# Optimization experiments

Hardware: AMD Instinct MI355X
Metric: run time of the kernel (lower is better)

## Reference

```python
import jax, jax.numpy as jnp
import numpy as np

N_NODES = 100_000
N_FACES = 200_000
N_EDGES1 = 800_000
N_TRIP = 500_000
H = 64
GEO_IN = 10 + 2 * 23  # 56
N_INTER = 3
DEPTH = 3  # finaldepth; total SPNN layers = DEPTH + 1
PI = float(np.pi)
EPS = 1e-5


def setup_inputs() -> dict:
    key = jax.random.key(0)
    ks = jax.random.split(key, 12)
    s = 0.05
    input_feature = jax.random.normal(ks[0], (N_NODES, H), jnp.float32)
    coords = jax.random.normal(ks[1], (N_NODES, 3), jnp.float32)
    face_norm = jax.random.normal(ks[2], (N_FACES, 3), jnp.float32)
    face_x = jax.random.normal(ks[3], (N_FACES, 23), jnp.float32)
    edge_whichface = jax.random.randint(ks[4], (N_EDGES1,), 0, N_FACES)
    edge_index_2rd = jax.random.randint(ks[5], (3, N_TRIP), 0, N_NODES)
    edx_ij = jax.random.randint(ks[6], (N_TRIP,), 0, N_EDGES1)
    edx_rand = jax.random.randint(ks[7], (N_TRIP,), 0, N_EDGES1)
    edx_jk = jnp.where(jnp.arange(N_TRIP) % 2 == 0, edx_ij, edx_rand)
    att = jnp.ones((2,), jnp.float32)
    W_geo = jax.random.normal(ks[8], (H, GEO_IN), jnp.float32) * s
    b_geo = jnp.zeros((H,), jnp.float32)
    g_geo = jnp.ones((H,), jnp.float32)
    be_geo = jnp.zeros((H,), jnp.float32)
    spnn_W0 = jax.random.normal(ks[9], (N_INTER, 2, H, 4 * H), jnp.float32) * s
    spnn_b0 = jnp.zeros((N_INTER, 2, H), jnp.float32)
    spnn_Wr = jax.random.normal(ks[10], (N_INTER, 2, DEPTH, H, H), jnp.float32) * s
    spnn_br = jnp.zeros((N_INTER, 2, DEPTH, H), jnp.float32)
    bn_g = jnp.ones((N_INTER, 2, DEPTH + 1, H), jnp.float32)
    bn_b = jnp.zeros((N_INTER, 2, DEPTH + 1, H), jnp.float32)
    return dict(input_feature=input_feature, coords=coords, face_norm=face_norm,
                face_x=face_x, att=att, W_geo=W_geo, b_geo=b_geo, g_geo=g_geo,
                be_geo=be_geo, spnn_W0=spnn_W0, spnn_b0=spnn_b0, spnn_Wr=spnn_Wr,
                spnn_br=spnn_br, bn_g=bn_g, bn_b=bn_b,
                edge_whichface=edge_whichface, edge_index_2rd=edge_index_2rd,
                edx_jk=edx_jk, edx_ij=edx_ij)


def _bn(x, g, b):
    # BatchNorm1d, training mode (batch stats, biased variance)
    mean = x.mean(0)
    var = ((x - mean) ** 2).mean(0)
    return (x - mean) * jax.lax.rsqrt(var + EPS) * g + b


def _masked_bn(x, mf, g, b):
    # BatchNorm over only the masked rows (original code runs BN on x_i[mask]);
    # applied to all rows, masked rows selected afterward -> identical math.
    cnt = jnp.maximum(mf.sum(), 1.0)
    mean = (x * mf).sum(0) / cnt
    var = (((x - mean) ** 2) * mf).sum(0) / cnt
    return (x - mean) * jax.lax.rsqrt(var + EPS) * g + b


def _angle(v1, v2):
    c = jnp.cross(v1, v2)
    return jnp.arctan2(jnp.linalg.norm(c, axis=1), (v1 * v2).sum(1))


def reference(input_feature, coords, face_norm, face_x, att, W_geo, b_geo,
              g_geo, be_geo, spnn_W0, spnn_b0, spnn_Wr, spnn_br, bn_g, bn_b,
              edge_whichface, edge_index_2rd, edx_jk, edx_ij):
    i, j, k = edge_index_2rd
    f_ij = edge_whichface[edx_ij]
    f_jk = edge_whichface[edx_jk]
    # angle_face is computed then multiplied by 0 in the original
    angle_face = (PI - _angle(face_norm[f_ij], face_norm[f_jk])) * 0.0
    cj, ci, ck = coords[j], coords[i], coords[k]
    d_ij = jnp.linalg.norm(cj - ci, axis=1)
    d_jk = jnp.linalg.norm(cj - ck, axis=1)
    theta = _angle(cj - ci, ck - cj)
    same_face = f_ij == f_jk
    geo = jnp.concatenate([d_ij[:, None], d_jk[:, None], theta[:, None],
                           angle_face[:, None], cj, ci,
                           face_x[f_ij], face_x[f_jk]], axis=-1)  # [E, 56]
    geo = jax.nn.relu(_bn(geo @ W_geo.T + b_geo, g_geo, be_geo))  # [E, H]

    nf = input_feature
    masks = [same_face, ~same_face]
    outs = []
    for t in range(N_INTER):
        xcat = jnp.concatenate([nf[i], nf[j], nf[k], geo], axis=-1)  # [E, 4H]
        x_out = jnp.zeros((xcat.shape[0], H), xcat.dtype)
        for bi in range(2):
            mf = masks[bi].astype(xcat.dtype)[:, None]
            x = jax.nn.relu(_masked_bn(xcat @ spnn_W0[t, bi].T + spnn_b0[t, bi],
                                       mf, bn_g[t, bi, 0], bn_b[t, bi, 0]))
            for l in range(DEPTH):
                x = jax.nn.relu(_masked_bn(x @ spnn_Wr[t, bi, l].T + spnn_br[t, bi, l],
                                           mf, bn_g[t, bi, l + 1], bn_b[t, bi, l + 1]))
            x = jax.nn.leaky_relu(x) * att[bi]
            x_out = x_out + x * mf
        nf = jax.ops.segment_sum(x_out, i, num_segments=N_NODES)
        outs.append(nf)
    return jnp.stack(outs)  # [N_INTER, N, H] (list in original)
```

## Files before the change

### kernel.cpp

```cpp
#include <hip/hip_runtime.h>

#define E_TRIP 500000
#define EPAD   500224
#define NTILE64 (EPAD/64)
#define NBLK256 (EPAD/256)
#define NBLK    1954
#define NN 100000
#define NBIN (2*NN)
#define EPSF 1e-5f
#define RSTAT 64

typedef _Float16 f16;
typedef _Float16 f16x8 __attribute__((ext_vector_type(8)));
typedef float f32x4 __attribute__((ext_vector_type(4)));

__global__ __launch_bounds__(256) void k_count(const int* __restrict__ ewf,
    const int* __restrict__ exij, const int* __restrict__ exjk,
    unsigned char* __restrict__ biedge, int* __restrict__ cb0)
{
  __shared__ int wcnt[4];
  int e = blockIdx.x*256 + threadIdx.x;
  bool active = e < E_TRIP;
  int b = 0;
  if (active) {
    int fij = ewf[exij[e]];
    int fjk = ewf[exjk[e]];
    b = (fij == fjk) ? 0 : 1;
    biedge[e] = (unsigned char)b;
  }
  unsigned long long m0 = __ballot(active && b==0);
  int lane = threadIdx.x & 63, wv = threadIdx.x >> 6;
  if (lane == 0) wcnt[wv] = (int)__popcll(m0);
  __syncthreads();
  if (threadIdx.x == 0) cb0[blockIdx.x] = wcnt[0] + wcnt[1] + wcnt[2] + wcnt[3];
}

__global__ __launch_bounds__(1024) void k_scanb(const int* __restrict__ cb0, int* __restrict__ sc)
{
  __shared__ int s[2048];
  int tid = threadIdx.x;
  int i0 = tid, i1 = tid + 1024;
  s[i0] = (i0 < NBLK) ? cb0[i0] : 0;
  s[i1] = (i1 < NBLK) ? cb0[i1] : 0;
  __syncthreads();
  for (int off = 1; off < 2048; off <<= 1) {
    int v0 = (i0 >= off) ? s[i0 - off] : 0;
    int v1 = (i1 >= off) ? s[i1 - off] : 0;
    __syncthreads();
    s[i0] += v0; s[i1] += v1;
    __syncthreads();
  }
  if (tid == 0) {
    int c0 = s[NBLK-1];
    int c0p = (c0 + 63) & ~63;
    sc[4] = c0; sc[5] = c0p; sc[6] = E_TRIP - c0;
  }
}

__global__ __launch_bounds__(256) void k_cvt(const float* __restrict__ W0,
    const float* __restrict__ Wr, const float* __restrict__ nf,
    f16* __restrict__ W0h, f16* __restrict__ Wrh, f16* __restrict__ nfh)
{
  int i = (blockIdx.x*256 + threadIdx.x) * 4;
  if (i < 98304) {
    float4 v = *(const float4*)(W0 + i);
    W0h[i]=(f16)v.x; W0h[i+1]=(f16)v.y; W0h[i+2]=(f16)v.z; W0h[i+3]=(f16)v.w;
  } else if (i < 172032) {
    int j = i - 98304;
    float4 v = *(const float4*)(Wr + j);
    Wrh[j]=(f16)v.x; Wrh[j+1]=(f16)v.y; Wrh[j+2]=(f16)v.z; Wrh[j+3]=(f16)v.w;
  } else {
    int j = i - 172032;
    if (j < NN*64) {
      float4 v = *(const float4*)(nf + j);
      nfh[j]=(f16)v.x; nfh[j+1]=(f16)v.y; nfh[j+2]=(f16)v.z; nfh[j+3]=(f16)v.w;
    }
  }
}

__global__ __launch_bounds__(256) void k_hist(const unsigned char* __restrict__ biedge,
    const int* __restrict__ eidx, int* __restrict__ cnt)
{
  int e = blockIdx.x*256 + threadIdx.x;
  if (e < E_TRIP) {
    int key = (int)biedge[e]*NN + eidx[e];
    atomicAdd(&cnt[key], 1);
  }
}

__global__ __launch_bounds__(512) void k_scan1(const int* __restrict__ cnt,
    int* __restrict__ start, int* __restrict__ btot)
{
  __shared__ int s[512];
  int tid = threadIdx.x;
  int g = blockIdx.x*512 + tid;
  int x = (g < NBIN) ? cnt[g] : 0;
  s[tid] = x; __syncthreads();
  #pragma unroll
  for (int off = 1; off < 512; off <<= 1) {
    int v = (tid >= off) ? s[tid-off] : 0;
    __syncthreads();
    s[tid] += v;
    __syncthreads();
  }
  if (g < NBIN) start[g] = s[tid] - x;
  if (tid == 511) btot[blockIdx.x] = s[511];
}

__global__ __launch_bounds__(512) void k_scan2(int* __restrict__ btot)
{
  __shared__ int s[512];
  int tid = threadIdx.x;
  int x = (tid < 391) ? btot[tid] : 0;
  s[tid] = x; __syncthreads();
  #pragma unroll
  for (int off = 1; off < 512; off <<= 1) {
    int v = (tid >= off) ? s[tid-off] : 0;
    __syncthreads();
    s[tid] += v;
    __syncthreads();
  }
  if (tid < 391) btot[tid] = s[tid] - x;
}

__global__ __launch_bounds__(512) void k_scan3(int* __restrict__ start,
    int* __restrict__ cur, const int* __restrict__ btot, const int* __restrict__ sc)
{
  int tid = threadIdx.x;
  int g = blockIdx.x*512 + tid;
  if (g < NBIN) {
    int v = start[g] + btot[blockIdx.x];
    if (g >= NN) v += sc[5] - sc[4];
    start[g] = v;
    cur[g] = v;
  }
  if (g == 0) start[NBIN] = sc[5] + sc[6];
}

__global__ __launch_bounds__(256) void k_place(const unsigned char* __restrict__ biedge,
    const int* __restrict__ eidx, int* __restrict__ cur,
    int* __restrict__ epos, int* __restrict__ ip, int* __restrict__ jp, int* __restrict__ kp)
{
  int e = blockIdx.x*256 + threadIdx.x;
  if (e < E_TRIP) {
    int i = eidx[e];
    int key = (int)biedge[e]*NN + i;
    int pos = atomicAdd(&cur[key], 1);
    epos[pos] = e;
    ip[pos] = i;
    jp[pos] = eidx[E_TRIP + e];
    kp[pos] = eidx[2*E_TRIP + e];
  }
}

__global__ __launch_bounds__(256) void k_geo(
    const float* __restrict__ coords, const float* __restrict__ facex,
    const int* __restrict__ ewf, const int* __restrict__ exij, const int* __restrict__ exjk,
    const float* __restrict__ Wgeo, const float* __restrict__ bgeo,
    const int* __restrict__ sc, const int* __restrict__ epos,
    const int* __restrict__ ip, const int* __restrict__ jp, const int* __restrict__ kp,
    f16* __restrict__ zgeo, float* __restrict__ gstats)
{
  __shared__ f16 lds[256*72];
  __shared__ float sstat[64][2];
  int tid = threadIdx.x;
  int base = blockIdx.x*256;
  int c0 = sc[4], c0p = sc[5], c1 = sc[6];
  if (tid < 128) ((float*)sstat)[tid] = 0.f;
  {
    int p = base + tid;
    bool valid = (p < c0) || (p >= c0p && p < c0p + c1);
    f16* lrow = lds + tid*72;
    if (valid) {
      int e = epos[p];
      int ii = ip[p], jj = jp[p], kk = kp[p];
      float cix = coords[ii*3+0], ciy = coords[ii*3+1], ciz = coords[ii*3+2];
      float cjx = coords[jj*3+0], cjy = coords[jj*3+1], cjz = coords[jj*3+2];
      float ckx = coords[kk*3+0], cky = coords[kk*3+1], ckz = coords[kk*3+2];
      float v1x = cjx-cix, v1y = cjy-ciy, v1z = cjz-ciz;
      float v2x = ckx-cjx, v2y = cky-cjy, v2z = ckz-cjz;
      float dij = sqrtf(v1x*v1x + v1y*v1y + v1z*v1z);
      float djk = sqrtf(v2x*v2x + v2y*v2y + v2z*v2z);
      float cx = v1y*v2z - v1z*v2y;
      float cy = v1z*v2x - v1x*v2z;
      float cz = v1x*v2y - v1y*v2x;
      float theta = atan2f(sqrtf(cx*cx+cy*cy+cz*cz), v1x*v2x+v1y*v2y+v1z*v2z);
      lrow[0]=(f16)dij; lrow[1]=(f16)djk; lrow[2]=(f16)theta; lrow[3]=(f16)0.f;
      lrow[4]=(f16)cjx; lrow[5]=(f16)cjy; lrow[6]=(f16)cjz;
      lrow[7]=(f16)cix; lrow[8]=(f16)ciy; lrow[9]=(f16)ciz;
      int fij = ewf[exij[e]], fjk = ewf[exjk[e]];
      const float* fx1 = facex + (size_t)fij*23;
      const float* fx2 = facex + (size_t)fjk*23;
      for (int c = 0; c < 23; c++) lrow[10+c] = (f16)fx1[c];
      for (int c = 0; c < 23; c++) lrow[33+c] = (f16)fx2[c];
      for (int c = 56; c < 64; c++) lrow[c] = (f16)0.f;
    } else {
      for (int c = 0; c < 64; c++) lrow[c] = (f16)0.f;
    }
  }
  __syncthreads();
  int wv = tid>>6, lane = tid&63, lg = lane>>4, lr = lane&15;
  f16x8 Bf[4][2];
  #pragma unroll
  for (int nt = 0; nt < 4; nt++) {
    #pragma unroll
    for (int ks = 0; ks < 2; ks++) {
      int n = nt*16 + lr;
      int kb = ks*32 + lg*8;
      f16x8 w;
      if (kb < 56) {
        float4 w0 = *(const float4*)(Wgeo + n*56 + kb);
        float4 w1 = *(const float4*)(Wgeo + n*56 + kb + 4);
        w[0]=(f16)w0.x; w[1]=(f16)w0.y; w[2]=(f16)w0.z; w[3]=(f16)w0.w;
        w[4]=(f16)w1.x; w[5]=(f16)w1.y; w[6]=(f16)w1.z; w[7]=(f16)w1.w;
      } else {
        #pragma unroll
        for (int j2 = 0; j2 < 8; j2++) w[j2] = (f16)0.f;
      }
      Bf[nt][ks] = w;
    }
  }
  float ssum[4] = {0,0,0,0}, ssq[4] = {0,0,0,0};
  for (int mt = 0; mt < 4; mt++) {
    int rbase = wv*64 + mt*16;
    f16x8 A0 = *(const f16x8*)(lds + (rbase+lr)*72 + lg*8);
    f16x8 A1 = *(const f16x8*)(lds + (rbase+lr)*72 + 32 + lg*8);
    f32x4 acc[4];
    #pragma unroll
    for (int nt = 0; nt < 4; nt++) { acc[nt][0]=0.f; acc[nt][1]=0.f; acc[nt][2]=0.f; acc[nt][3]=0.f; }
    #pragma unroll
    for (int nt = 0; nt < 4; nt++) {
      acc[nt] = __builtin_amdgcn_mfma_f32_16x16x32_f16(A0, Bf[nt][0], acc[nt], 0, 0, 0);
      acc[nt] = __builtin_amdgcn_mfma_f32_16x16x32_f16(A1, Bf[nt][1], acc[nt], 0, 0, 0);
    }
    #pragma unroll
    for (int nt = 0; nt < 4; nt++) {
      int n = nt*16 + lr;
      float bg = bgeo[n];
      #pragma unroll
      for (int rg = 0; rg < 4; rg++) {
        int rloc = rbase + lg*4 + rg;
        int p = base + rloc;
        bool valid = (p < c0) || (p >= c0p && p < c0p + c1);
        float z = valid ? (acc[nt][rg] + bg) : 0.f;
        ssum[nt] += z; ssq[nt] += z*z;
        lds[rloc*72 + n] = (f16)z;
      }
    }
  }
  #pragma unroll
  for (int nt = 0; nt < 4; nt++) {
    float v = ssum[nt]; v += __shfl_xor(v, 16); v += __shfl_xor(v, 32);
    float w = ssq[nt];  w += __shfl_xor(w, 16); w += __shfl_xor(w, 32);
    if (lane < 16) { atomicAdd(&sstat[nt*16+lane][0], v); atomicAdd(&sstat[nt*16+lane][1], w); }
  }
  __syncthreads();
  {
    int p = base + tid;
    #pragma unroll
    for (int c = 0; c < 8; c++) {
      f16x8 v = *(const f16x8*)(lds + tid*72 + c*8);
      *(f16x8*)(zgeo + (size_t)p*64 + c*8) = v;
    }
  }
  if (tid < 128) {
    float v = ((float*)sstat)[tid];
    if (v != 0.f) atomicAdd(&gstats[(blockIdx.x & (RSTAT-1))*256 + tid], v);
  }
}

__global__ __launch_bounds__(256) void k_geobn(f16* __restrict__ zg,
    const float* __restrict__ g_geo, const float* __restrict__ be_geo,
    const float* __restrict__ gstats)
{
  __shared__ float scale[64], shift[64];
  int tid = threadIdx.x;
  if (tid < 64) {
    float s = 0.f, sq = 0.f;
    #pragma unroll 8
    for (int r = 0; r < RSTAT; r++) {
      s  += gstats[r*256 + tid*2];
      sq += gstats[r*256 + tid*2 + 1];
    }
    float mean = s * (1.f/(float)E_TRIP);
    float var  = sq * (1.f/(float)E_TRIP) - mean*mean;
    float rstd = rsqrtf(var + EPSF);
    float scl = g_geo[tid]*rstd;
    scale[tid] = scl;
    shift[tid] = be_geo[tid] - mean*scl;
  }
  __syncthreads();
  size_t idx = ((size_t)blockIdx.x*256 + tid) * 8;
  if (idx >= (size_t)EPAD*64) return;
  int f0 = (int)(idx & 63);
  f16x8 raw = *(const f16x8*)(zg + idx);
  f16x8 u;
  #pragma unroll
  for (int j2 = 0; j2 < 8; j2++) {
    float x = fmaxf((float)raw[j2]*scale[f0+j2] + shift[f0+j2], 0.f);
    u[j2] = (f16)x;
  }
  *(f16x8*)(zg + idx) = u;
}

__global__ __launch_bounds__(256) void k_layer0(
    const f16* __restrict__ nfsrc, const f16* __restrict__ zgbn,
    const f16* __restrict__ W0p, const float* __restrict__ b0p,
    float* __restrict__ outstats,
    const int* __restrict__ sc, const int* __restrict__ ip,
    const int* __restrict__ jp, const int* __restrict__ kp,
    f16* __restrict__ z0)
{
  __shared__ f16 lds[64*200];
  __shared__ float sstat[2][64][2];
  int tid = threadIdx.x;
  int c0 = sc[4], c0p = sc[5], c1 = sc[6];
  ((float*)sstat)[tid] = 0.f;
  __syncthreads();
  int wv = tid>>6, lane = tid&63, lg = lane>>4, lr = lane&15;
  float s0sum[4]={0,0,0,0}, s0sq[4]={0,0,0,0}, s1sum[4]={0,0,0,0}, s1sq[4]={0,0,0,0};
  for (int tile = blockIdx.x; tile < NTILE64; tile += gridDim.x) {
    int rowbase = tile*64;
    int branch = (rowbase >= c0p) ? 1 : 0;
    int pr = rowbase + wv*16 + lr;
    f16x8 G0 = *(const f16x8*)(zgbn + (size_t)pr*64 + lg*8);
    f16x8 G1 = *(const f16x8*)(zgbn + (size_t)pr*64 + 32 + lg*8);
    {
      int r = tid >> 2, q = tid & 3;
      if (q < 3) {
        int p = rowbase + r;
        bool valid = (p < c0) || (p >= c0p && p < c0p + c1);
        f16* rowp = lds + r*200 + q*64;
        if (valid) {
          int idx = (q==0 ? ip : (q==1 ? jp : kp))[p];
          const f16* src = nfsrc + (size_t)idx*64;
          #pragma unroll
          for (int c = 0; c < 8; c++) *(f16x8*)(rowp + c*8) = *(const f16x8*)(src + c*8);
        } else {
          f16x8 u;
          #pragma unroll
          for (int j2 = 0; j2 < 8; j2++) u[j2] = (f16)0.f;
          #pragma unroll
          for (int c = 0; c < 8; c++) *(f16x8*)(rowp + c*8) = u;
        }
      }
    }
    __syncthreads();
    {
      int r0 = wv*16;
      const f16* Wb = W0p + branch*16384;
      f32x4 acc[4];
      #pragma unroll
      for (int nt = 0; nt < 4; nt++) { acc[nt][0]=0.f; acc[nt][1]=0.f; acc[nt][2]=0.f; acc[nt][3]=0.f; }
      #pragma unroll
      for (int ks = 0; ks < 6; ks++) {
        f16x8 A = *(const f16x8*)(lds + (r0+lr)*200 + ks*32 + lg*8);
        #pragma unroll
        for (int nt = 0; nt < 4; nt++) {
          f16x8 B = *(const f16x8*)(Wb + (nt*16+lr)*256 + ks*32 + lg*8);
          acc[nt] = __builtin_amdgcn_mfma_f32_16x16x32_f16(A, B, acc[nt], 0, 0, 0);
        }
      }
      #pragma unroll
      for (int nt = 0; nt < 4; nt++) {
        f16x8 B0 = *(const f16x8*)(Wb + (nt*16+lr)*256 + 192 + lg*8);
        acc[nt] = __builtin_amdgcn_mfma_f32_16x16x32_f16(G0, B0, acc[nt], 0, 0, 0);
        f16x8 B1 = *(const f16x8*)(Wb + (nt*16+lr)*256 + 224 + lg*8);
        acc[nt] = __builtin_amdgcn_mfma_f32_16x16x32_f16(G1, B1, acc[nt], 0, 0, 0);
      }
      __syncthreads();
      #pragma unroll
      for (int nt = 0; nt < 4; nt++) {
        int n = nt*16 + lr;
        float bias = b0p[branch*64 + n];
        #pragma unroll
        for (int rg = 0; rg < 4; rg++) {
          int rloc = r0 + lg*4 + rg;
          int p = rowbase + rloc;
          bool valid = (p < c0) || (p >= c0p && p < c0p + c1);
          float z = valid ? (acc[nt][rg] + bias) : 0.f;
          if (branch == 0) { s0sum[nt] += z; s0sq[nt] += z*z; }
          else             { s1sum[nt] += z; s1sq[nt] += z*z; }
          lds[rloc*200 + n] = (f16)z;
        }
      }
    }
    __syncthreads();
    {
      int r = tid>>2, q = tid&3;
      int p = rowbase + r;
      f16x8 v0 = *(const f16x8*)(lds + r*200 + q*16);
      f16x8 v1 = *(const f16x8*)(lds + r*200 + q*16 + 8);
      *(f16x8*)(z0 + (size_t)p*64 + q*16) = v0;
      *(f16x8*)(z0 + (size_t)p*64 + q*16 + 8) = v1;
    }
    __syncthreads();
  }
  #pragma unroll
  for (int nt = 0; nt < 4; nt++) {
    float v, w;
    v = s0sum[nt]; v += __shfl_xor(v,16); v += __shfl_xor(v,32);
    w = s0sq[nt];  w += __shfl_xor(w,16); w += __shfl_xor(w,32);
    if (lane < 16) { atomicAdd(&sstat[0][nt*16+lane][0], v); atomicAdd(&sstat[0][nt*16+lane][1], w); }
    v = s1sum[nt]; v += __shfl_xor(v,16); v += __shfl_xor(v,32);
    w = s1sq[nt];  w += __shfl_xor(w,16); w += __shfl_xor(w,32);
    if (lane < 16) { atomicAdd(&sstat[1][nt*16+lane][0], v); atomicAdd(&sstat[1][nt*16+lane][1], w); }
  }
  __syncthreads();
  {
    float v = ((float*)sstat)[tid];
    if (v != 0.f) atomicAdd(&outstats[(blockIdx.x & (RSTAT-1))*256 + tid], v);
  }
}

__global__ __launch_bounds__(256) void k_hidden(
    const f16* __restrict__ zin, f16* __restrict__ zout,
    const f16* __restrict__ Wp, const float* __restrict__ biasp,
    const float* __restrict__ bngp, const float* __restrict__ bnbp,
    const float* __restrict__ instats, float* __restrict__ outstats,
    const int* __restrict__ sc)
{
  __shared__ float lscale[2][64], lshift[2][64];
  __shared__ float sstat[2][64][2];
  __shared__ f16 ldso[4][16*72];
  int tid = threadIdx.x;
  int c0 = sc[4], c0p = sc[5], c1 = sc[6];
  if (tid < 128) {
    int b = tid>>6, n = tid&63;
    int cb = b ? c1 : c0; if (cb < 1) cb = 1;
    float inv = 1.f/(float)cb;
    int idx = (b*64+n)*2;
    float s = 0.f, sq = 0.f;
    #pragma unroll 8
    for (int r = 0; r < RSTAT; r++) {
      s  += instats[r*256 + idx];
      sq += instats[r*256 + idx + 1];
    }
    float mean = s*inv, var = sq*inv - mean*mean;
    float rstd = rsqrtf(var + EPSF);
    float scl = bngp[b*256+n]*rstd;
    lscale[b][n] = scl;
    lshift[b][n] = bnbp[b*256+n] - mean*scl;
  }
  ((float*)sstat)[tid] = 0.f;
  __syncthreads();
  int wv = tid>>6, lane = tid&63, lg = lane>>4, lr = lane&15;
  f16* myldso = ldso[wv];
  float s0sum[4]={0,0,0,0}, s0sq[4]={0,0,0,0}, s1sum[4]={0,0,0,0}, s1sq[4]={0,0,0,0};
  for (int tile = blockIdx.x; tile < NTILE64; tile += gridDim.x) {
    int rowbase = tile*64;
    int branch = (rowbase >= c0p) ? 1 : 0;
    int rgl = rowbase + wv*16 + lr;
    f16x8 Af[2];
    #pragma unroll
    for (int ks = 0; ks < 2; ks++) {
      f16x8 raw = *(const f16x8*)(zin + (size_t)rgl*64 + ks*32 + lg*8);
      f16x8 A;
      #pragma unroll
      for (int j2 = 0; j2 < 8; j2++) {
        int f = ks*32 + lg*8 + j2;
        float x = fmaxf((float)raw[j2]*lscale[branch][f] + lshift[branch][f], 0.f);
        A[j2] = (f16)x;
      }
      Af[ks] = A;
    }
    f32x4 acc[4];
    #pragma unroll
    for (int nt = 0; nt < 4; nt++) { acc[nt][0]=0.f; acc[nt][1]=0.f; acc[nt][2]=0.f; acc[nt][3]=0.f; }
    #pragma unroll
    for (int ks = 0; ks < 2; ks++) {
      #pragma unroll
      for (int nt = 0; nt < 4; nt++) {
        f16x8 B = *(const f16x8*)(Wp + branch*12288 + (nt*16+lr)*64 + ks*32 + lg*8);
        acc[nt] = __builtin_amdgcn_mfma_f32_16x16x32_f16(Af[ks], B, acc[nt], 0, 0, 0);
      }
    }
    #pragma unroll
    for (int nt = 0; nt < 4; nt++) {
      int n = nt*16 + lr;
      float bias = biasp[branch*192 + n];
      #pragma unroll
      for (int rg = 0; rg < 4; rg++) {
        int rloc = lg*4 + rg;
        int p = rowbase + wv*16 + rloc;
        bool valid = (p < c0) || (p >= c0p && p < c0p + c1);
        float z = valid ? (acc[nt][rg] + bias) : 0.f;
        if (branch == 0) { s0sum[nt] += z; s0sq[nt] += z*z; }
        else             { s1sum[nt] += z; s1sq[nt] += z*z; }
        myldso[rloc*72 + n] = (f16)z;
      }
    }
    {
      int r2 = lane>>2, q = lane&3;
      int p2 = rowbase + wv*16 + r2;
      f16x8 v0 = *(const f16x8*)(myldso + r2*72 + q*8);
      f16x8 v1 = *(const f16x8*)(myldso + r2*72 + 32 + q*8);
      *(f16x8*)(zout + (size_t)p2*64 + q*8) = v0;
      *(f16x8*)(zout + (size_t)p2*64 + 32 + q*8) = v1;
    }
  }
  #pragma unroll
  for (int nt = 0; nt < 4; nt++) {
    float v, w;
    v = s0sum[nt]; v += __shfl_xor(v,16); v += __shfl_xor(v,32);
    w = s0sq[nt];  w += __shfl_xor(w,16); w += __shfl_xor(w,32);
    if (lane < 16) { atomicAdd(&sstat[0][nt*16+lane][0], v); atomicAdd(&sstat[0][nt*16+lane][1], w); }
    v = s1sum[nt]; v += __shfl_xor(v,16); v += __shfl_xor(v,32);
    w = s1sq[nt];  w += __shfl_xor(w,16); w += __shfl_xor(w,32);
    if (lane < 16) { atomicAdd(&sstat[1][nt*16+lane][0], v); atomicAdd(&sstat[1][nt*16+lane][1], w); }
  }
  __syncthreads();
  {
    float v = ((float*)sstat)[tid];
    if (v != 0.f) atomicAdd(&outstats[(blockIdx.x & (RSTAT-1))*256 + tid], v);
  }
}

__global__ __launch_bounds__(256) void k_scatter(
    const f16* __restrict__ z3, const float* __restrict__ att,
    const float* __restrict__ bngp, const float* __restrict__ bnbp,
    const float* __restrict__ instats, const int* __restrict__ sc,
    const int* __restrict__ astart,
    float* __restrict__ outt, f16* __restrict__ nfh)
{
  __shared__ float lscale[2][64], lshift[2][64];
  int tid = threadIdx.x;
  int c0 = sc[4];
  {
    if (tid < 128) {
      int b = tid>>6, n = tid&63;
      int cb = b ? sc[6] : sc[4]; if (cb < 1) cb = 1;
      float inv = 1.f/(float)cb;
      int idx = (b*64+n)*2;
      float s = 0.f, sq = 0.f;
      #pragma unroll 8
      for (int r = 0; r < RSTAT; r++) {
        s  += instats[r*256 + idx];
        sq += instats[r*256 + idx + 1];
      }
      float mean = s*inv, var = sq*inv - mean*mean;
      float rstd = rsqrtf(var + EPSF);
      float scl = bngp[b*256+n]*rstd;
      lscale[b][n] = scl;
      lshift[b][n] = bnbp[b*256+n] - mean*scl;
    }
  }
  __syncthreads();
  int gid = blockIdx.x*256 + tid;
  int n = gid >> 3, q = gid & 7;
  if (n >= NN) return;
  int s0 = astart[n];
  int e0 = astart[n+1]; if (e0 > c0) e0 = c0;
  int s1 = astart[NN+n];
  int e1 = astart[NN+n+1];
  float a0 = att[0], a1 = att[1];
  float acc[8] = {0,0,0,0,0,0,0,0};
  float scb[8], shb[8];
  #pragma unroll
  for (int j2 = 0; j2 < 8; j2++) { scb[j2] = lscale[0][q*8+j2]; shb[j2] = lshift[0][q*8+j2]; }
  for (int t = s0; t < e0; t++) {
    f16x8 raw = *(const f16x8*)(z3 + (size_t)t*64 + q*8);
    #pragma unroll
    for (int j2 = 0; j2 < 8; j2++) {
      float x = (float)raw[j2]*scb[j2] + shb[j2];
      acc[j2] += fmaxf(x, 0.f) * a0;
    }
  }
  #pragma unroll
  for (int j2 = 0; j2 < 8; j2++) { scb[j2] = lscale[1][q*8+j2]; shb[j2] = lshift[1][q*8+j2]; }
  for (int t = s1; t < e1; t++) {
    f16x8 raw = *(const f16x8*)(z3 + (size_t)t*64 + q*8);
    #pragma unroll
    for (int j2 = 0; j2 < 8; j2++) {
      float x = (float)raw[j2]*scb[j2] + shb[j2];
      acc[j2] += fmaxf(x, 0.f) * a1;
    }
  }
  float4 lo, hi;
  lo.x=acc[0]; lo.y=acc[1]; lo.z=acc[2]; lo.w=acc[3];
  hi.x=acc[4]; hi.y=acc[5]; hi.z=acc[6]; hi.w=acc[7];
  *(float4*)(outt + (size_t)n*64 + q*8) = lo;
  *(float4*)(outt + (size_t)n*64 + q*8 + 4) = hi;
  f16x8 h;
  #pragma unroll
  for (int j2 = 0; j2 < 8; j2++) h[j2] = (f16)acc[j2];
  *(f16x8*)(nfh + (size_t)n*64 + q*8) = h;
}

extern "C" void kernel_launch(void* const* d_in, const int* in_sizes, int n_in,
                              void* d_out, int out_size, void* d_ws, size_t ws_size,
                              hipStream_t stream)
{
  const float* input_feature = (const float*)d_in[0];
  const float* coords   = (const float*)d_in[1];
  const float* face_x   = (const float*)d_in[3];
  const float* att      = (const float*)d_in[4];
  const float* W_geo    = (const float*)d_in[5];
  const float* b_geo    = (const float*)d_in[6];
  const float* g_geo    = (const float*)d_in[7];
  const float* be_geo   = (const float*)d_in[8];
  const float* spnn_W0  = (const float*)d_in[9];
  const float* spnn_b0  = (const float*)d_in[10];
  const float* spnn_Wr  = (const float*)d_in[11];
  const float* spnn_br  = (const float*)d_in[12];
  const float* bn_g     = (const float*)d_in[13];
  const float* bn_b     = (const float*)d_in[14];
  const int* ewf  = (const int*)d_in[15];
  const int* eidx = (const int*)d_in[16];
  const int* exjk = (const int*)d_in[17];
  const int* exij = (const int*)d_in[18];
  float* out = (float*)d_out;
  char* ws = (char*)d_ws;

  size_t off = 0;
  auto take = [&](size_t bytes) -> char* {
    size_t o = off; off = (off + bytes + 255) & ~(size_t)255; return ws + o;
  };
  const size_t STATBUF = (size_t)RSTAT*256;
  int*   sc     = (int*)take(256);
  float* stats  = (float*)take(13*STATBUF*sizeof(float));
  int*   cb0    = (int*)take(sizeof(int)*2048);
  int*   cnt    = (int*)take(sizeof(int)*NBIN);
  int*   astart = (int*)take(sizeof(int)*(NBIN+1));
  int*   curn   = (int*)take(sizeof(int)*NBIN);
  int*   btot   = (int*)take(sizeof(int)*512);
  unsigned char* biedge = (unsigned char*)take(E_TRIP);
  int* epos = (int*)take(sizeof(int)*EPAD);
  int* ip   = (int*)take(sizeof(int)*EPAD);
  int* jp   = (int*)take(sizeof(int)*EPAD);
  int* kp   = (int*)take(sizeof(int)*EPAD);
  f16* W0h  = (f16*)take(sizeof(f16)*3*2*64*256);
  f16* Wrh  = (f16*)take(sizeof(f16)*3*2*3*64*64);
  f16* nf16 = (f16*)take(sizeof(f16)*(size_t)NN*64);
  f16* zgeo = (f16*)take(sizeof(f16)*(size_t)EPAD*64);
  f16* zA   = (f16*)take(sizeof(f16)*(size_t)EPAD*64);
  f16* zB   = (f16*)take(sizeof(f16)*(size_t)EPAD*64);
  if (off > ws_size) return;

  hipMemsetAsync(sc, 0, 256, stream);
  hipMemsetAsync(stats, 0, 13*STATBUF*sizeof(float), stream);
  hipMemsetAsync(cnt, 0, sizeof(int)*NBIN, stream);

  k_count <<<NBLK, 256, 0, stream>>>(ewf, exij, exjk, biedge, cb0);
  k_scanb <<<1, 1024, 0, stream>>>(cb0, sc);
  k_cvt   <<<6418, 256, 0, stream>>>(spnn_W0, spnn_Wr, input_feature, W0h, Wrh, nf16);
  k_hist  <<<NBLK, 256, 0, stream>>>(biedge, eidx, cnt);
  k_scan1 <<<391, 512, 0, stream>>>(cnt, astart, btot);
  k_scan2 <<<1, 512, 0, stream>>>(btot);
  k_scan3 <<<391, 512, 0, stream>>>(astart, curn, btot, sc);
  k_place <<<NBLK, 256, 0, stream>>>(biedge, eidx, curn, epos, ip, jp, kp);

  k_geo   <<<NBLK256, 256, 0, stream>>>(coords, face_x, ewf, exij, exjk, W_geo, b_geo,
                                        sc, epos, ip, jp, kp, zgeo, stats);
  k_geobn <<<(EPAD*64/8 + 255)/256, 256, 0, stream>>>(zgeo, g_geo, be_geo, stats);
  for (int t = 0; t < 3; t++) {
    float* outt = out + (size_t)t*NN*64;
    k_layer0<<<1954, 256, 0, stream>>>(nf16, zgeo,
        W0h + (size_t)t*2*64*256, spnn_b0 + t*2*64,
        stats + (size_t)(1 + t*4)*STATBUF,
        sc, ip, jp, kp, zA);
    f16* zi = zA; f16* zo = zB;
    for (int h = 0; h < 3; h++) {
      k_hidden<<<1954, 256, 0, stream>>>(zi, zo,
          Wrh + (size_t)t*2*3*64*64 + (size_t)h*64*64,
          spnn_br + t*2*3*64 + h*64,
          bn_g + t*2*4*64 + h*64,
          bn_b + t*2*4*64 + h*64,
          stats + (size_t)(1 + t*4 + h)*STATBUF,
          stats + (size_t)(1 + t*4 + h + 1)*STATBUF,
          sc);
      f16* tmp = zi; zi = zo; zo = tmp;
    }
    k_scatter<<<(NN*8 + 255)/256, 256, 0, stream>>>(zi, att,
        bn_g + t*2*4*64 + 3*64, bn_b + t*2*4*64 + 3*64,
        stats + (size_t)(1 + t*4 + 3)*STATBUF, sc, astart, outt, nf16);
  }
}
```

Baseline: 1.416 ms.

## Fuse hidden SPNN layers and scatter into persistent kernel with grid barriers

Replaces the three k_hidden launches and the k_scatter launch per interaction with one persistent kernel of 768 blocks. Each block keeps its 11 row tiles in registers across the three hidden layers and uses a software grid barrier to finalize batch-norm statistics between layers. This avoids the intermediate activation round-trips to global memory and the launch gaps. The cost is heavy register pressure, reliance on all 768 blocks being co-resident for the spin barrier (it has a timeout escape), and a scatter phase run on fewer blocks.

```diff
diff --git a/kernel.cpp b/kernel.cpp
--- a/kernel.cpp
+++ b/kernel.cpp
@@ -9,6 +9,8 @@
 #define NBIN (2*NN)
 #define EPSF 1e-5f
 #define RSTAT 64
+#define GRID_F 768
+#define SLOTS 11
 
 typedef _Float16 f16;
 typedef _Float16 f16x8 __attribute__((ext_vector_type(8)));
@@ -413,178 +415,208 @@
   }
 }
 
-__global__ __launch_bounds__(256) void k_hidden(
-    const f16* __restrict__ zin, f16* __restrict__ zout,
-    const f16* __restrict__ Wp, const float* __restrict__ biasp,
-    const float* __restrict__ bngp, const float* __restrict__ bnbp,
-    const float* __restrict__ instats, float* __restrict__ outstats,
-    const int* __restrict__ sc)
-{
+__device__ __forceinline__ void gridbar(int* bar)
+{
+  __syncthreads();
+  if (threadIdx.x == 0) {
+    __threadfence();
+    int g = __hip_atomic_load(&bar[1], __ATOMIC_RELAXED, __HIP_MEMORY_SCOPE_AGENT);
+    int a = __hip_atomic_fetch_add(&bar[0], 1, __ATOMIC_ACQ_REL, __HIP_MEMORY_SCOPE_AGENT);
+    if (a == GRID_F-1) {
+      __hip_atomic_store(&bar[0], 0, __ATOMIC_RELAXED, __HIP_MEMORY_SCOPE_AGENT);
+      __hip_atomic_fetch_add(&bar[1], 1, __ATOMIC_RELEASE, __HIP_MEMORY_SCOPE_AGENT);
+    } else {
+      int iter = 0;
+      while (__hip_atomic_load(&bar[1], __ATOMIC_ACQUIRE, __HIP_MEMORY_SCOPE_AGENT) == g) {
+        __builtin_amdgcn_s_sleep(32);
+        if (++iter > (1<<20)) break;
+      }
+    }
+    __threadfence();
+  }
+  __syncthreads();
+}
+
+__global__ __launch_bounds__(256, 3) void k_fused(
+    const f16* __restrict__ z0, const f16* __restrict__ Wr,
+    const float* __restrict__ brp, const float* __restrict__ bngt,
+    const float* __restrict__ bnbt, const float* __restrict__ att,
+    const float* __restrict__ instats0, float* __restrict__ stats1,
+    float* __restrict__ stats2, float* __restrict__ stats3,
+    const int* __restrict__ sc, const int* __restrict__ astart,
+    f16* __restrict__ z3, float* __restrict__ outt, f16* __restrict__ nfh,
+    int* __restrict__ bar)
+{
+  __shared__ f16 ldst[4][16*72];
   __shared__ float lscale[2][64], lshift[2][64];
-  __shared__ float sstat[2][64][2];
-  __shared__ f16 ldso[4][16*72];
+  __shared__ float sstat[256];
   int tid = threadIdx.x;
+  int wv = tid>>6, lane = tid&63, lg = lane>>4, lr = lane&15;
   int c0 = sc[4], c0p = sc[5], c1 = sc[6];
+  f16* myldst = ldst[wv];
+
   if (tid < 128) {
     int b = tid>>6, n = tid&63;
     int cb = b ? c1 : c0; if (cb < 1) cb = 1;
     float inv = 1.f/(float)cb;
-    int idx = (b*64+n)*2;
     float s = 0.f, sq = 0.f;
     #pragma unroll 8
     for (int r = 0; r < RSTAT; r++) {
-      s  += instats[r*256 + idx];
-      sq += instats[r*256 + idx + 1];
+      s  += instats0[r*256 + (b*64+n)*2];
+      sq += instats0[r*256 + (b*64+n)*2 + 1];
     }
     float mean = s*inv, var = sq*inv - mean*mean;
     float rstd = rsqrtf(var + EPSF);
-    float scl = bngp[b*256+n]*rstd;
+    float scl = bngt[b*256 + n]*rstd;
     lscale[b][n] = scl;
-    lshift[b][n] = bnbp[b*256+n] - mean*scl;
-  }
-  ((float*)sstat)[tid] = 0.f;
-  __syncthreads();
-  int wv = tid>>6, lane = tid&63, lg = lane>>4, lr = lane&15;
-  f16* myldso = ldso[wv];
-  float s0sum[4]={0,0,0,0}, s0sq[4]={0,0,0,0}, s1sum[4]={0,0,0,0}, s1sq[4]={0,0,0,0};
-  for (int tile = blockIdx.x; tile < NTILE64; tile += gridDim.x) {
-    int rowbase = tile*64;
-    int branch = (rowbase >= c0p) ? 1 : 0;
-    int rgl = rowbase + wv*16 + lr;
-    f16x8 Af[2];
+    lshift[b][n] = bnbt[b*256 + n] - mean*scl;
+  }
+  __syncthreads();
+
+  f16x8 za[SLOTS], zb[SLOTS];
+  #pragma unroll
+  for (int s = 0; s < SLOTS; s++) {
+    int tile = blockIdx.x + s*GRID_F;
+    if (tile < NTILE64) {
+      int rgl = tile*64 + wv*16 + lr;
+      za[s] = *(const f16x8*)(z0 + (size_t)rgl*64 + lg*8);
+      zb[s] = *(const f16x8*)(z0 + (size_t)rgl*64 + 32 + lg*8);
+    } else {
+      #pragma unroll
+      for (int j2 = 0; j2 < 8; j2++) { za[s][j2] = (f16)0.f; zb[s][j2] = (f16)0.f; }
+    }
+  }
+
+  for (int h = 0; h < 3; h++) {
+    float* outstats = (h==0) ? stats1 : (h==1) ? stats2 : stats3;
+    sstat[tid] = 0.f;
+    __syncthreads();
+    float s0s[4]={0,0,0,0}, s0q[4]={0,0,0,0}, s1s[4]={0,0,0,0}, s1q[4]={0,0,0,0};
     #pragma unroll
-    for (int ks = 0; ks < 2; ks++) {
-      f16x8 raw = *(const f16x8*)(zin + (size_t)rgl*64 + ks*32 + lg*8);
-      f16x8 A;
-      #pragma unroll
-      for (int j2 = 0; j2 < 8; j2++) {
-        int f = ks*32 + lg*8 + j2;
-        float x = fmaxf((float)raw[j2]*lscale[branch][f] + lshift[branch][f], 0.f);
-        A[j2] = (f16)x;
-      }
-      Af[ks] = A;
-    }
-    f32x4 acc[4];
-    #pragma unroll
-    for (int nt = 0; nt < 4; nt++) { acc[nt][0]=0.f; acc[nt][1]=0.f; acc[nt][2]=0.f; acc[nt][3]=0.f; }
-    #pragma unroll
-    for (int ks = 0; ks < 2; ks++) {
-      #pragma unroll
-      for (int nt = 0; nt < 4; nt++) {
-        f16x8 B = *(const f16x8*)(Wp + branch*12288 + (nt*16+lr)*64 + ks*32 + lg*8);
-        acc[nt] = __builtin_amdgcn_mfma_f32_16x16x32_f16(Af[ks], B, acc[nt], 0, 0, 0);
+    for (int s = 0; s < SLOTS; s++) {
+      int tile = blockIdx.x + s*GRID_F;
+      if (tile < NTILE64) {
+        int rowbase = tile*64;
+        int branch = (rowbase >= c0p) ? 1 : 0;
+        f16x8 A0, A1;
+        #pragma unroll
+        for (int j2 = 0; j2 < 8; j2++) {
+          int f0 = lg*8 + j2;
+          A0[j2] = (f16)fmaxf((float)za[s][j2]*lscale[branch][f0] + lshift[branch][f0], 0.f);
+          int f1 = 32 + lg*8 + j2;
+          A1[j2] = (f16)fmaxf((float)zb[s][j2]*lscale[branch][f1] + lshift[branch][f1], 0.f);
+        }
+        const f16* Wb = Wr + branch*12288 + h*4096;
+        f32x4 acc[4];
+        #pragma unroll
+        for (int nt = 0; nt < 4; nt++) { acc[nt][0]=0.f; acc[nt][1]=0.f; acc[nt][2]=0.f; acc[nt][3]=0.f; }
+        #pragma unroll
+        for (int nt = 0; nt < 4; nt++) {
+          f16x8 B0 = *(const f16x8*)(Wb + (nt*16+lr)*64 + lg*8);
+          acc[nt] = __builtin_amdgcn_mfma_f32_16x16x32_f16(A0, B0, acc[nt], 0, 0, 0);
+          f16x8 B1 = *(const f16x8*)(Wb + (nt*16+lr)*64 + 32 + lg*8);
+          acc[nt] = __builtin_amdgcn_mfma_f32_16x16x32_f16(A1, B1, acc[nt], 0, 0, 0);
+        }
+        #pragma unroll
+        for (int nt = 0; nt < 4; nt++) {
+          int n = nt*16 + lr;
+          float bias = brp[branch*192 + h*64 + n];
+          #pragma unroll
+          for (int rg = 0; rg < 4; rg++) {
+            int rloc = lg*4 + rg;
+            int p = rowbase + wv*16 + rloc;
+            bool valid = (p < c0) || (p >= c0p && p < c0p + c1);
+            float z = valid ? (acc[nt][rg] + bias) : 0.f;
+            if (branch) { s1s[nt] += z; s1q[nt] += z*z; } else { s0s[nt] += z; s0q[nt] += z*z; }
+            myldst[rloc*72 + n] = (f16)z;
+          }
+        }
+        za[s] = *(const f16x8*)(myldst + lr*72 + lg*8);
+        zb[s] = *(const f16x8*)(myldst + lr*72 + 32 + lg*8);
+        if (h == 2) {
+          int pr = rowbase + wv*16 + lr;
+          *(f16x8*)(z3 + (size_t)pr*64 + lg*8) = za[s];
+          *(f16x8*)(z3 + (size_t)pr*64 + 32 + lg*8) = zb[s];
+        }
       }
     }
     #pragma unroll
     for (int nt = 0; nt < 4; nt++) {
-      int n = nt*16 + lr;
-      float bias = biasp[branch*192 + n];
-      #pragma unroll
-      for (int rg = 0; rg < 4; rg++) {
-        int rloc = lg*4 + rg;
-        int p = rowbase + wv*16 + rloc;
-        bool valid = (p < c0) || (p >= c0p && p < c0p + c1);
-        float z = valid ? (acc[nt][rg] + bias) : 0.f;
-        if (branch == 0) { s0sum[nt] += z; s0sq[nt] += z*z; }
-        else             { s1sum[nt] += z; s1sq[nt] += z*z; }
-        myldso[rloc*72 + n] = (f16)z;
-      }
-    }
+      float v, w;
+      v = s0s[nt]; v += __shfl_xor(v,16); v += __shfl_xor(v,32);
+      w = s0q[nt]; w += __shfl_xor(w,16); w += __shfl_xor(w,32);
+      if (lane < 16) { atomicAdd(&sstat[(nt*16+lane)*2], v); atomicAdd(&sstat[(nt*16+lane)*2+1], w); }
+      v = s1s[nt]; v += __shfl_xor(v,16); v += __shfl_xor(v,32);
+      w = s1q[nt]; w += __shfl_xor(w,16); w += __shfl_xor(w,32);
+      if (lane < 16) { atomicAdd(&sstat[128+(nt*16+lane)*2], v); atomicAdd(&sstat[128+(nt*16+lane)*2+1], w); }
+    }
+    __syncthreads();
     {
-      int r2 = lane>>2, q = lane&3;
-      int p2 = rowbase + wv*16 + r2;
-      f16x8 v0 = *(const f16x8*)(myldso + r2*72 + q*8);
-      f16x8 v1 = *(const f16x8*)(myldso + r2*72 + 32 + q*8);
-      *(f16x8*)(zout + (size_t)p2*64 + q*8) = v0;
-      *(f16x8*)(zout + (size_t)p2*64 + 32 + q*8) = v1;
-    }
-  }
-  #pragma unroll
-  for (int nt = 0; nt < 4; nt++) {
-    float v, w;
-    v = s0sum[nt]; v += __shfl_xor(v,16); v += __shfl_xor(v,32);
-    w = s0sq[nt];  w += __shfl_xor(w,16); w += __shfl_xor(w,32);
-    if (lane < 16) { atomicAdd(&sstat[0][nt*16+lane][0], v); atomicAdd(&sstat[0][nt*16+lane][1], w); }
-    v = s1sum[nt]; v += __shfl_xor(v,16); v += __shfl_xor(v,32);
-    w = s1sq[nt];  w += __shfl_xor(w,16); w += __shfl_xor(w,32);
-    if (lane < 16) { atomicAdd(&sstat[1][nt*16+lane][0], v); atomicAdd(&sstat[1][nt*16+lane][1], w); }
-  }
-  __syncthreads();
-  {
-    float v = ((float*)sstat)[tid];
-    if (v != 0.f) atomicAdd(&outstats[(blockIdx.x & (RSTAT-1))*256 + tid], v);
-  }
-}
-
-__global__ __launch_bounds__(256) void k_scatter(
-    const f16* __restrict__ z3, const float* __restrict__ att,
-    const float* __restrict__ bngp, const float* __restrict__ bnbp,
-    const float* __restrict__ instats, const int* __restrict__ sc,
-    const int* __restrict__ astart,
-    float* __restrict__ outt, f16* __restrict__ nfh)
-{
-  __shared__ float lscale[2][64], lshift[2][64];
-  int tid = threadIdx.x;
-  int c0 = sc[4];
-  {
+      float v = sstat[tid];
+      if (v != 0.f) atomicAdd(&outstats[(blockIdx.x & (RSTAT-1))*256 + tid], v);
+    }
+    gridbar(bar);
     if (tid < 128) {
       int b = tid>>6, n = tid&63;
-      int cb = b ? sc[6] : sc[4]; if (cb < 1) cb = 1;
+      int cb = b ? c1 : c0; if (cb < 1) cb = 1;
       float inv = 1.f/(float)cb;
-      int idx = (b*64+n)*2;
       float s = 0.f, sq = 0.f;
       #pragma unroll 8
       for (int r = 0; r < RSTAT; r++) {
-        s  += instats[r*256 + idx];
-        sq += instats[r*256 + idx + 1];
+        s  += __hip_atomic_load(&outstats[r*256 + (b*64+n)*2], __ATOMIC_RELAXED, __HIP_MEMORY_SCOPE_AGENT);
+        sq += __hip_atomic_load(&outstats[r*256 + (b*64+n)*2 + 1], __ATOMIC_RELAXED, __HIP_MEMORY_SCOPE_AGENT);
       }
       float mean = s*inv, var = sq*inv - mean*mean;
       float rstd = rsqrtf(var + EPSF);
-      float scl = bngp[b*256+n]*rstd;
+      int l = h + 1;
+      float scl = bngt[b*256 + l*64 + n]*rstd;
       lscale[b][n] = scl;
-      lshift[b][n] = bnbp[b*256+n] - mean*scl;
-    }
-  }
-  __syncthreads();
-  int gid = blockIdx.x*256 + tid;
-  int n = gid >> 3, q = gid & 7;
-  if (n >= NN) return;
-  int s0 = astart[n];
-  int e0 = astart[n+1]; if (e0 > c0) e0 = c0;
-  int s1 = astart[NN+n];
-  int e1 = astart[NN+n+1];
-  float a0 = att[0], a1 = att[1];
-  float acc[8] = {0,0,0,0,0,0,0,0};
-  float scb[8], shb[8];
-  #pragma unroll
-  for (int j2 = 0; j2 < 8; j2++) { scb[j2] = lscale[0][q*8+j2]; shb[j2] = lshift[0][q*8+j2]; }
-  for (int t = s0; t < e0; t++) {
-    f16x8 raw = *(const f16x8*)(z3 + (size_t)t*64 + q*8);
-    #pragma unroll
-    for (int j2 = 0; j2 < 8; j2++) {
-      float x = (float)raw[j2]*scb[j2] + shb[j2];
-      acc[j2] += fmaxf(x, 0.f) * a0;
-    }
-  }
-  #pragma unroll
-  for (int j2 = 0; j2 < 8; j2++) { scb[j2] = lscale[1][q*8+j2]; shb[j2] = lshift[1][q*8+j2]; }
-  for (int t = s1; t < e1; t++) {
-    f16x8 raw = *(const f16x8*)(z3 + (size_t)t*64 + q*8);
-    #pragma unroll
-    for (int j2 = 0; j2 < 8; j2++) {
-      float x = (float)raw[j2]*scb[j2] + shb[j2];
-      acc[j2] += fmaxf(x, 0.f) * a1;
-    }
-  }
-  float4 lo, hi;
-  lo.x=acc[0]; lo.y=acc[1]; lo.z=acc[2]; lo.w=acc[3];
-  hi.x=acc[4]; hi.y=acc[5]; hi.z=acc[6]; hi.w=acc[7];
-  *(float4*)(outt + (size_t)n*64 + q*8) = lo;
-  *(float4*)(outt + (size_t)n*64 + q*8 + 4) = hi;
-  f16x8 h;
-  #pragma unroll
-  for (int j2 = 0; j2 < 8; j2++) h[j2] = (f16)acc[j2];
-  *(f16x8*)(nfh + (size_t)n*64 + q*8) = h;
+      lshift[b][n] = bnbt[b*256 + l*64 + n] - mean*scl;
+    }
+    __syncthreads();
+  }
+
+  {
+    float a0 = att[0], a1 = att[1];
+    for (int gid = blockIdx.x*256 + tid; gid < NN*8; gid += GRID_F*256) {
+      int n = gid >> 3, q = gid & 7;
+      int s0 = astart[n];
+      int e0 = astart[n+1]; if (e0 > c0) e0 = c0;
+      int s1 = astart[NN+n];
+      int e1 = astart[NN+n+1];
+      float acc[8] = {0,0,0,0,0,0,0,0};
+      float scb[8], shb[8];
+      #pragma unroll
+      for (int j2 = 0; j2 < 8; j2++) { scb[j2] = lscale[0][q*8+j2]; shb[j2] = lshift[0][q*8+j2]; }
+      for (int t = s0; t < e0; t++) {
+        f16x8 raw = *(const f16x8*)(z3 + (size_t)t*64 + q*8);
+        #pragma unroll
+        for (int j2 = 0; j2 < 8; j2++) {
+          float x = (float)raw[j2]*scb[j2] + shb[j2];
+          acc[j2] += fmaxf(x, 0.f) * a0;
+        }
+      }
+      #pragma unroll
+      for (int j2 = 0; j2 < 8; j2++) { scb[j2] = lscale[1][q*8+j2]; shb[j2] = lshift[1][q*8+j2]; }
+      for (int t = s1; t < e1; t++) {
+        f16x8 raw = *(const f16x8*)(z3 + (size_t)t*64 + q*8);
+        #pragma unroll
+        for (int j2 = 0; j2 < 8; j2++) {
+          float x = (float)raw[j2]*scb[j2] + shb[j2];
+          acc[j2] += fmaxf(x, 0.f) * a1;
+        }
+      }
+      float4 lo, hi;
+      lo.x=acc[0]; lo.y=acc[1]; lo.z=acc[2]; lo.w=acc[3];
+      hi.x=acc[4]; hi.y=acc[5]; hi.z=acc[6]; hi.w=acc[7];
+      *(float4*)(outt + (size_t)n*64 + q*8) = lo;
+      *(float4*)(outt + (size_t)n*64 + q*8 + 4) = hi;
+      f16x8 hh;
+      #pragma unroll
+      for (int j2 = 0; j2 < 8; j2++) hh[j2] = (f16)acc[j2];
+      *(f16x8*)(nfh + (size_t)n*64 + q*8) = hh;
+    }
+  }
 }
 
 extern "C" void kernel_launch(void* const* d_in, const int* in_sizes, int n_in,
@@ -618,6 +650,7 @@
   };
   const size_t STATBUF = (size_t)RSTAT*256;
   int*   sc     = (int*)take(256);
+  int*   bar    = (int*)take(256);
   float* stats  = (float*)take(13*STATBUF*sizeof(float));
   int*   cb0    = (int*)take(sizeof(int)*2048);
   int*   cnt    = (int*)take(sizeof(int)*NBIN);
@@ -637,7 +670,7 @@
   f16* zB   = (f16*)take(sizeof(f16)*(size_t)EPAD*64);
   if (off > ws_size) return;
 
-  hipMemsetAsync(sc, 0, 256, stream);
+  hipMemsetAsync(sc, 0, 512, stream);
   hipMemsetAsync(stats, 0, 13*STATBUF*sizeof(float), stream);
   hipMemsetAsync(cnt, 0, sizeof(int)*NBIN, stream);
 
@@ -659,20 +692,14 @@
         W0h + (size_t)t*2*64*256, spnn_b0 + t*2*64,
         stats + (size_t)(1 + t*4)*STATBUF,
         sc, ip, jp, kp, zA);
-    f16* zi = zA; f16* zo = zB;
-    for (int h = 0; h < 3; h++) {
-      k_hidden<<<1954, 256, 0, stream>>>(zi, zo,
-          Wrh + (size_t)t*2*3*64*64 + (size_t)h*64*64,
-          spnn_br + t*2*3*64 + h*64,
-          bn_g + t*2*4*64 + h*64,
-          bn_b + t*2*4*64 + h*64,
-          stats + (size_t)(1 + t*4 + h)*STATBUF,
-          stats + (size_t)(1 + t*4 + h + 1)*STATBUF,
-          sc);
-      f16* tmp = zi; zi = zo; zo = tmp;
-    }
-    k_scatter<<<(NN*8 + 255)/256, 256, 0, stream>>>(zi, att,
-        bn_g + t*2*4*64 + 3*64, bn_b + t*2*4*64 + 3*64,
-        stats + (size_t)(1 + t*4 + 3)*STATBUF, sc, astart, outt, nf16);
-  }
-}
+    k_fused<<<GRID_F, 256, 0, stream>>>(zA,
+        Wrh + (size_t)t*2*3*64*64,
+        spnn_br + t*2*3*64,
+        bn_g + t*2*4*64, bn_b + t*2*4*64, att,
+        stats + (size_t)(1 + t*4)*STATBUF,
+        stats + (size_t)(2 + t*4)*STATBUF,
+        stats + (size_t)(3 + t*4)*STATBUF,
+        stats + (size_t)(4 + t*4)*STATBUF,
+        sc, astart, zB, outt, nf16, bar);
+  }
+}
```

Measured after the change: 2.553 ms. 80.2% more time.
